# Optimization experiments

Hardware: AMD Instinct MI355X
Metric: run time of the kernel (lower is better)

## Reference

```python
import jax, jax.numpy as jnp
import numpy as np

S, N_SUB, E_SUB = 64, 1024, 16384       # subgraphs, nodes/subgraph, edges/subgraph
N, E = 65536, 1048576                   # global nodes / edges
F_IN, NHID, NCLS, HEADS = 128, 128, 64, 2
RATIO = 0.5
K = int(np.ceil(RATIO * N_SUB))         # SAGPooling keeps K=512 nodes


def setup_inputs() -> dict:
    key = jax.random.key(0)
    ks = jax.random.split(key, 12)
    def lin(k, i, o):
        return jax.random.normal(k, (i, o), jnp.float32) / np.sqrt(i).astype(np.float32)
    return {
        'sub_x': jax.random.normal(ks[0], (S, N_SUB, F_IN), jnp.float32),
        'sub_edge_index': jax.random.randint(ks[1], (S, 2, E_SUB), 0, N_SUB, jnp.int32),
        'sub_orig_idx': jax.random.randint(ks[2], (S, N_SUB), 0, N, jnp.int32),
        'edge_index': jax.random.randint(ks[3], (2, E), 0, N, jnp.int32),
        'W1': lin(ks[4], F_IN, NHID), 'b1': jnp.zeros((NHID,), jnp.float32),
        'W2': lin(ks[5], NHID, NHID), 'b2': jnp.zeros((NHID,), jnp.float32),
        'Wp': lin(ks[6], NHID, 1), 'bp': jnp.zeros((1,), jnp.float32),
        'Wsc': lin(ks[7], NHID, NHID), 'bsc': jnp.zeros((NHID,), jnp.float32),
        'Wqkv': lin(ks[8], 2 * NHID, 6 * NHID), 'bqkv': jnp.zeros((6 * NHID,), jnp.float32),
        'Wo': lin(ks[9], 2 * NHID, 2 * NHID), 'bo': jnp.zeros((2 * NHID,), jnp.float32),
        'Wf': lin(ks[10], 3 * NHID, NCLS), 'bf': jnp.zeros((NCLS,), jnp.float32),
    }


def gcn(x, src, dst, ew, W, b, n):
    """PyG GCNConv: sym-normalized aggregation with self-loops; ew masks invalid edges."""
    h = x @ W
    deg = jax.ops.segment_sum(ew, dst, num_segments=n) + 1.0  # +1 self-loop
    dinv = jax.lax.rsqrt(deg)
    coef = dinv[src] * dinv[dst] * ew
    agg = jax.ops.segment_sum(h[src] * coef[:, None], dst, num_segments=n)
    return agg + h * (dinv * dinv)[:, None] + b


def _forward(sub_x, W1, b1, W2, b2, Wp, bp, Wsc, bsc, Wqkv, bqkv, Wo, bo, Wf, bf,
             sub_edge_index, sub_orig_idx, edge_index):
    dt = sub_x.dtype

    def cacos(x, ei):  # one subgraph: [N_SUB,F], [2,E_SUB]
        src, dst = ei[0], ei[1]
        ew1 = jnp.ones((E_SUB,), dt)
        x1 = jax.nn.relu(gcn(x, src, dst, ew1, W1, b1, N_SUB))
        x2 = jax.nn.relu(gcn(x1, src, dst, ew1, W2, b2, N_SUB))
        # SAGPooling on x1: GCN scorer -> top-k -> tanh gate
        score = gcn(x1, src, dst, ew1, Wp, bp, N_SUB)[:, 0]
        top_s, perm = jax.lax.top_k(score, K)
        x_pool = x1[perm] * jnp.tanh(top_s)[:, None]
        # remap edges to pooled indexing; invalid edges get weight 0
        pos = jnp.full((N_SUB,), -1, jnp.int32).at[perm].set(jnp.arange(K, dtype=jnp.int32))
        valid = (pos[src] >= 0) & (pos[dst] >= 0)
        psrc = jnp.where(valid, pos[src], 0)
        pdst = jnp.where(valid, pos[dst], 0)
        ew2 = valid.astype(dt)
        emb1 = jnp.concatenate([x_pool.max(0), x_pool.mean(0)])  # [2*NHID]
        x_sub = jax.nn.relu(gcn(x_pool, psrc, pdst, ew2, Wsc, bsc, K))
        emb2 = jnp.concatenate([x_sub.max(0), x_sub.mean(0)])
        return x2, emb1 + emb2

    node_embs, sub_embs = jax.vmap(cacos)(sub_x, sub_edge_index)  # [S,N_SUB,NHID], [S,2*NHID]

    # multi-head self-attention over subgraph embeddings (seq_len = 1 per the torch reshape)
    HD = (2 * NHID) // HEADS
    qkv = (sub_embs @ Wqkv + bqkv).reshape(S, 1, 3, HEADS, HD).transpose(2, 0, 3, 1, 4)
    q, k, v = qkv[0], qkv[1], qkv[2]                      # [S,H,1,HD]
    attn = jax.nn.softmax(jnp.einsum('shqd,shkd->shqk', q, k) / np.sqrt(HD).astype(np.float32), axis=-1)
    o = jnp.einsum('shqk,shkd->shqd', attn, v).transpose(0, 2, 1, 3).reshape(S, 1, 2 * NHID)
    att = (o @ Wo + bo)[:, 0]                             # [S, 2*NHID]

    # scatter-add per-node embeddings + broadcast subgraph embedding into global buffer
    combined = jnp.concatenate(
        [node_embs, jnp.broadcast_to(att[:, None, :], (S, N_SUB, 2 * NHID))], axis=-1)
    global_emb = jnp.zeros((N, 3 * NHID), dt).at[sub_orig_idx.reshape(-1)].add(
        combined.reshape(-1, 3 * NHID))

    logits = gcn(global_emb, edge_index[0], edge_index[1], jnp.ones((E,), dt), Wf, bf, N)
    return jax.nn.log_softmax(logits, axis=-1), global_emb


def reference(sub_x, sub_edge_index, sub_orig_idx, edge_index, W1, b1, W2, b2, Wp, bp,
              Wsc, bsc, Wqkv, bqkv, Wo, bo, Wf, bf):
    return _forward(sub_x, W1, b1, W2, b2, Wp, bp, Wsc, bsc, Wqkv, bqkv, Wo, bo, Wf, bf,
                    sub_edge_index, sub_orig_idx, edge_index)
```

## Files before the change

kernel.cpp:

```cpp
#include <hip/hip_runtime.h>
#include <math.h>

#define S     64
#define NSUB  1024
#define ESUB  16384
#define NG    65536
#define EG    1048576
#define NH    128
#define KSEL  512
#define BCAP  20480

__global__ __launch_bounds__(1024) void k_csr_sub(const int* __restrict__ sei,
        const int* __restrict__ sorig, int* __restrict__ rowptr, int* __restrict__ col,
        float* __restrict__ dinv, int* __restrict__ cntR) {
    int b = blockIdx.x, t = threadIdx.x;
    if (b >= 64) {
        int r = (b - 64) * 1024 + t;
        atomicAdd(&cntR[sorig[r]], 1);
        return;
    }
    __shared__ int sh[1024];
    __shared__ int curL[1024];
    int s = b;
    curL[t] = 0;
    __syncthreads();
    const int* dstp = sei + s * 2 * ESUB + ESUB;
    #pragma unroll
    for (int k = 0; k < 16; k++) atomicAdd(&curL[dstp[k * 1024 + t]], 1);
    __syncthreads();
    int v = curL[t];
    sh[t] = v;
    __syncthreads();
    for (int off = 1; off < 1024; off <<= 1) {
        int add = (t >= off) ? sh[t - off] : 0;
        __syncthreads();
        sh[t] += add;
        __syncthreads();
    }
    int incl = sh[t];
    int excl = incl - v;
    rowptr[s * (NSUB + 1) + t] = excl;
    dinv[s * NSUB + t] = rsqrtf((float)(v + 1));
    if (t == 1023) rowptr[s * (NSUB + 1) + NSUB] = incl;
    curL[t] = s * ESUB + excl;
    __syncthreads();
    const int* srcp = sei + s * 2 * ESUB;
    #pragma unroll
    for (int k = 0; k < 16; k++) {
        int e = k * 1024 + t;
        int src = srcp[e];
        int dst = dstp[e];
        int p = atomicAdd(&curL[dst], 1);
        col[p] = src;
    }
}

__global__ __launch_bounds__(1024) void k_scanR(const int* __restrict__ cnt,
        int* __restrict__ rowptr, int* __restrict__ cur) {
    __shared__ int sh[1024];
    __shared__ int wsum[16];
    __shared__ int sboff;
    int b = blockIdx.x, t = threadIdx.x;
    int pre = 0;
    for (int i = t; i < b * 1024; i += 1024) pre += cnt[i];
    #pragma unroll
    for (int o = 32; o > 0; o >>= 1) pre += __shfl_xor(pre, o, 64);
    if ((t & 63) == 0) wsum[t >> 6] = pre;
    __syncthreads();
    if (t == 0) {
        int r = 0;
        #pragma unroll
        for (int i = 0; i < 16; i++) r += wsum[i];
        sboff = r;
    }
    int v = cnt[b * 1024 + t];
    sh[t] = v;
    __syncthreads();
    for (int off = 1; off < 1024; off <<= 1) {
        int add = (t >= off) ? sh[t - off] : 0;
        __syncthreads();
        sh[t] += add;
        __syncthreads();
    }
    int base = sboff;
    int r = base + sh[t] - v;
    int idx = b * 1024 + t;
    rowptr[idx] = r;
    cur[idx] = r;
    if (b == 63 && t == 1023) rowptr[NG] = base + sh[t];
}

__global__ void k_fillR(const int* __restrict__ orig, int* __restrict__ cur,
                        int* __restrict__ rowlist, int* __restrict__ posR) {
    int r = blockIdx.x * 256 + threadIdx.x;
    int p = atomicAdd(&cur[orig[r]], 1);
    rowlist[p] = r;
    posR[r] = p;
}

template<int KDIM, int NCOL>
__global__ __launch_bounds__(256) void k_matmul(const float* __restrict__ X,
        const float* __restrict__ W, float* __restrict__ Y) {
    __shared__ float As[16][72];
    __shared__ float Bs[16][72];
    int t = threadIdx.x;
    int row0 = blockIdx.x * 64;
    int col0 = blockIdx.y * 64;
    int tr = t >> 4, tc = t & 15;
    float acc[4][4] = {};
    for (int k0 = 0; k0 < KDIM; k0 += 16) {
        {   int r = t >> 2, kq = t & 3;
            float4 v = *(const float4*)&X[(size_t)(row0 + r) * KDIM + k0 + kq * 4];
            As[kq * 4 + 0][r] = v.x; As[kq * 4 + 1][r] = v.y;
            As[kq * 4 + 2][r] = v.z; As[kq * 4 + 3][r] = v.w;
        }
        {   int k = t >> 4, cq = t & 15;
            float4 v = *(const float4*)&W[(size_t)(k0 + k) * NCOL + col0 + cq * 4];
            *(float4*)&Bs[k][cq * 4] = v;
        }
        __syncthreads();
        #pragma unroll
        for (int k = 0; k < 16; k++) {
            float a0 = As[k][tr * 4 + 0], a1 = As[k][tr * 4 + 1];
            float a2 = As[k][tr * 4 + 2], a3 = As[k][tr * 4 + 3];
            float b0 = Bs[k][tc * 4 + 0], b1 = Bs[k][tc * 4 + 1];
            float b2 = Bs[k][tc * 4 + 2], b3 = Bs[k][tc * 4 + 3];
            acc[0][0] += a0 * b0; acc[0][1] += a0 * b1; acc[0][2] += a0 * b2; acc[0][3] += a0 * b3;
            acc[1][0] += a1 * b0; acc[1][1] += a1 * b1; acc[1][2] += a1 * b2; acc[1][3] += a1 * b3;
            acc[2][0] += a2 * b0; acc[2][1] += a2 * b1; acc[2][2] += a2 * b2; acc[2][3] += a2 * b3;
            acc[3][0] += a3 * b0; acc[3][1] += a3 * b1; acc[3][2] += a3 * b2; acc[3][3] += a3 * b3;
        }
        __syncthreads();
    }
    #pragma unroll
    for (int i = 0; i < 4; i++) {
        float4 v = { acc[i][0], acc[i][1], acc[i][2], acc[i][3] };
        *(float4*)&Y[(size_t)(row0 + tr * 4 + i) * NCOL + col0 + tc * 4] = v;
    }
}

__global__ __launch_bounds__(256) void k_mm2s(const float* __restrict__ X,
        const float* __restrict__ W, float* __restrict__ Y,
        const float* __restrict__ sh, const float* __restrict__ dinv,
        const int* __restrict__ rowptr, const int* __restrict__ col,
        const float* __restrict__ bp, float* __restrict__ score) {
    int t = threadIdx.x;
    if (blockIdx.x >= 2048) {
        int n = (blockIdx.x - 2048) * 256 + t;
        int s = n >> 10, nl = n & (NSUB - 1);
        const int* rp = rowptr + s * (NSUB + 1);
        const int* cl = col + s * ESUB;
        const float* dv = dinv + s * NSUB;
        int st = rp[nl], en = rp[nl + 1];
        float acc = 0.f;
        for (int p = st; p < en; p++) {
            int src = cl[p];
            acc += sh[s * NSUB + src] * dv[src];
        }
        float dn = dv[nl];
        score[n] = acc * dn + sh[n] * dn * dn + bp[0];
        return;
    }
    __shared__ float As[16][72];
    __shared__ float Bs[16][72];
    int row0 = (blockIdx.x & 1023) * 64;
    int col0 = (blockIdx.x >> 10) * 64;
    int tr = t >> 4, tc = t & 15;
    float acc[4][4] = {};
    for (int k0 = 0; k0 < 128; k0 += 16) {
        {   int r = t >> 2, kq = t & 3;
            float4 v = *(const float4*)&X[(size_t)(row0 + r) * 128 + k0 + kq * 4];
            As[kq * 4 + 0][r] = v.x; As[kq * 4 + 1][r] = v.y;
            As[kq * 4 + 2][r] = v.z; As[kq * 4 + 3][r] = v.w;
        }
        {   int k = t >> 4, cq = t & 15;
            float4 v = *(const float4*)&W[(size_t)(k0 + k) * 128 + col0 + cq * 4];
            *(float4*)&Bs[k][cq * 4] = v;
        }
        __syncthreads();
        #pragma unroll
        for (int k = 0; k < 16; k++) {
            float a0 = As[k][tr * 4 + 0], a1 = As[k][tr * 4 + 1];
            float a2 = As[k][tr * 4 + 2], a3 = As[k][tr * 4 + 3];
            float b0 = Bs[k][tc * 4 + 0], b1 = Bs[k][tc * 4 + 1];
            float b2 = Bs[k][tc * 4 + 2], b3 = Bs[k][tc * 4 + 3];
            acc[0][0] += a0 * b0; acc[0][1] += a0 * b1; acc[0][2] += a0 * b2; acc[0][3] += a0 * b3;
            acc[1][0] += a1 * b0; acc[1][1] += a1 * b1; acc[1][2] += a1 * b2; acc[1][3] += a1 * b3;
            acc[2][0] += a2 * b0; acc[2][1] += a2 * b1; acc[2][2] += a2 * b2; acc[2][3] += a2 * b3;
            acc[3][0] += a3 * b0; acc[3][1] += a3 * b1; acc[3][2] += a3 * b2; acc[3][3] += a3 * b3;
        }
        __syncthreads();
    }
    #pragma unroll
    for (int i = 0; i < 4; i++) {
        float4 v = { acc[i][0], acc[i][1], acc[i][2], acc[i][3] };
        *(float4*)&Y[(size_t)(row0 + tr * 4 + i) * 128 + col0 + tc * 4] = v;
    }
}

template<bool SCORE, bool SCATTER>
__global__ __launch_bounds__(256) void k_agg128(const float4* __restrict__ h,
        const float* __restrict__ dinv, const int* __restrict__ rowptr,
        const int* __restrict__ col, const float* __restrict__ bias,
        const float* __restrict__ Wp, const int* __restrict__ posR,
        float4* __restrict__ out, float* __restrict__ scoreh) {
    int b = blockIdx.x;
    int s = b & 63;
    int chunk = b >> 6;
    int t = threadIdx.x;
    int nl = chunk * 8 + (t >> 5);
    int f4 = t & 31;
    const int* rp = rowptr + s * (NSUB + 1);
    int st = rp[nl], en = rp[nl + 1];
    const int* cl = col + s * ESUB;
    const float* dv = dinv + s * NSUB;
    float4 acc = {0.f, 0.f, 0.f, 0.f};
    for (int p = st; p < en; p++) {
        int src = cl[p];
        float d = dv[src];
        float4 hv = h[((size_t)(s * NSUB + src)) * 32 + f4];
        acc.x += hv.x * d; acc.y += hv.y * d; acc.z += hv.z * d; acc.w += hv.w * d;
    }
    size_t node = (size_t)s * NSUB + nl;
    float dn = dv[nl];
    float dn2 = dn * dn;
    float4 hs = h[node * 32 + f4];
    float4 bb = ((const float4*)bias)[f4];
    float4 r;
    r.x = fmaxf(acc.x * dn + hs.x * dn2 + bb.x, 0.f);
    r.y = fmaxf(acc.y * dn + hs.y * dn2 + bb.y, 0.f);
    r.z = fmaxf(acc.z * dn + hs.z * dn2 + bb.z, 0.f);
    r.w = fmaxf(acc.w * dn + hs.w * dn2 + bb.w, 0.f);
    size_t orow = SCATTER ? (size_t)posR[node] : node;
    out[orow * 32 + f4] = r;
    if (SCORE) {
        float4 wp = ((const float4*)Wp)[f4];
        float p = r.x * wp.x + r.y * wp.y + r.z * wp.z + r.w * wp.w;
        #pragma unroll
        for (int o = 16; o > 0; o >>= 1) p += __shfl_xor(p, o, 32);
        if (f4 == 0) scoreh[node] = p;
    }
}

__global__ __launch_bounds__(512) void k_topk(const float* __restrict__ score,
        int* __restrict__ perm, float* __restrict__ gate, int* __restrict__ posmap) {
    __shared__ float sv[1024];
    __shared__ int   si[1024];
    int s = blockIdx.x, t = threadIdx.x;
    for (int i = t; i < 1024; i += 512) {
        sv[i] = score[s * NSUB + i];
        si[i] = i;
        posmap[s * NSUB + i] = -1;
    }
    __syncthreads();
    for (int k = 2; k <= 1024; k <<= 1) {
        for (int j = k >> 1; j > 0; j >>= 1) {
            for (int b = t; b < 1024; b += 512) {
                int ixj = b ^ j;
                if (ixj > b) {
                    bool desc = ((b & k) == 0);
                    bool sw = desc ? (sv[b] < sv[ixj]) : (sv[b] > sv[ixj]);
                    if (sw) {
                        float tv = sv[b]; sv[b] = sv[ixj]; sv[ixj] = tv;
                        int ti = si[b]; si[b] = si[ixj]; si[ixj] = ti;
                    }
                }
            }
            __syncthreads();
        }
    }
    if (t < KSEL) {
        perm[s * KSEL + t] = si[t];
        gate[s * KSEL + t] = tanhf(sv[t]);
        posmap[s * NSUB + si[t]] = t;
    }
}

__global__ __launch_bounds__(256) void k_pool(const float4* __restrict__ x1,
        const int* __restrict__ perm, const float* __restrict__ gate,
        const int* __restrict__ posmap, const int* __restrict__ rowptr,
        const int* __restrict__ col, float* __restrict__ dinv2,
        float4* __restrict__ xpool) {
    int t = threadIdx.x;
    int i = blockIdx.x * 8 + (t >> 5);
    int lane = t & 31;
    int s = i >> 9;
    int n = perm[i];
    const int* rp = rowptr + s * (NSUB + 1);
    const int* cl = col + s * ESUB;
    int st = rp[n], en = rp[n + 1];
    int c = 0;
    for (int p = st + lane; p < en; p += 32) c += (posmap[s * NSUB + cl[p]] >= 0) ? 1 : 0;
    #pragma unroll
    for (int o = 16; o > 0; o >>= 1) c += __shfl_xor(c, o, 32);
    if (lane == 0) dinv2[i] = rsqrtf((float)(c + 1));
    float g = gate[i];
    float4 v = x1[((size_t)(s * NSUB + n)) * 32 + lane];
    v.x *= g; v.y *= g; v.z *= g; v.w *= g;
    xpool[(size_t)i * 32 + lane] = v;
}

__global__ __launch_bounds__(1024) void k_emb(const float* __restrict__ X,
        float* __restrict__ out) {
    __shared__ float red[4][256];
    int s = blockIdx.x, t = threadIdx.x;
    int sl = t >> 8, f = t & 255;
    const float* base = X + (size_t)s * KSEL * NH;
    float r;
    if (f < NH) {
        r = -INFINITY;
        for (int i = sl * 128; i < sl * 128 + 128; i++) r = fmaxf(r, base[i * NH + f]);
    } else {
        r = 0.f;
        for (int i = sl * 128; i < sl * 128 + 128; i++) r += base[i * NH + (f - NH)];
    }
    red[sl][f] = r;
    __syncthreads();
    if (sl == 0) {
        float a = red[0][f], b = red[1][f], c = red[2][f], d = red[3][f];
        float v = (f < NH) ? fmaxf(fmaxf(a, b), fmaxf(c, d)) : (a + b + c + d) * (1.f / KSEL);
        out[s * 256 + f] = v;
    }
}

__global__ __launch_bounds__(256) void k_aggp_bin(const float4* __restrict__ hp,
        const float* __restrict__ dinv2, const int* __restrict__ perm,
        const int* __restrict__ posmap, const int* __restrict__ rowptr,
        const int* __restrict__ col, const float* __restrict__ bsc,
        float4* __restrict__ xsub,
        const int* __restrict__ gei, int* __restrict__ bcur, int* __restrict__ ebin) {
    int t = threadIdx.x;
    if (blockIdx.x >= 4096) {
        __shared__ int lh[64];
        __shared__ int lbase[64];
        if (t < 64) lh[t] = 0;
        __syncthreads();
        int e0 = (blockIdx.x - 4096) * 8192;
        #pragma unroll 8
        for (int k = 0; k < 32; k++) {
            int d = gei[EG + e0 + k * 256 + t];
            atomicAdd(&lh[d >> 10], 1);
        }
        __syncthreads();
        if (t < 64) {
            lbase[t] = t * BCAP + atomicAdd(&bcur[t], lh[t]);
            lh[t] = 0;
        }
        __syncthreads();
        #pragma unroll 4
        for (int k = 0; k < 32; k++) {
            int idx = e0 + k * 256 + t;
            int d = gei[EG + idx];
            int src = gei[idx];
            int bb = d >> 10;
            int pos = lbase[bb] + atomicAdd(&lh[bb], 1);
            ebin[pos] = src | ((d & 1023) << 16);
        }
        return;
    }
    int b = blockIdx.x;
    int s = b & 63;
    int chunk = b >> 6;
    int il = chunk * 8 + (t >> 5);
    int f4 = t & 31;
    int i = s * KSEL + il;
    int n = perm[i];
    const int* rp = rowptr + s * (NSUB + 1);
    const int* cl = col + s * ESUB;
    int st = rp[n], en = rp[n + 1];
    float4 acc = {0.f, 0.f, 0.f, 0.f};
    for (int p = st; p < en; p++) {
        int j = posmap[s * NSUB + cl[p]];
        if (j >= 0) {
            float d = dinv2[s * KSEL + j];
            float4 hv = hp[((size_t)(s * KSEL + j)) * 32 + f4];
            acc.x += hv.x * d; acc.y += hv.y * d; acc.z += hv.z * d; acc.w += hv.w * d;
        }
    }
    float dn = dinv2[i];
    float dn2 = dn * dn;
    float4 hs = hp[(size_t)i * 32 + f4];
    float4 bb = ((const float4*)bsc)[f4];
    float4 r;
    r.x = fmaxf(acc.x * dn + hs.x * dn2 + bb.x, 0.f);
    r.y = fmaxf(acc.y * dn + hs.y * dn2 + bb.y, 0.f);
    r.z = fmaxf(acc.z * dn + hs.z * dn2 + bb.z, 0.f);
    r.w = fmaxf(acc.w * dn + hs.w * dn2 + bb.w, 0.f);
    xsub[(size_t)i * 32 + f4] = r;
}

__global__ __launch_bounds__(1024) void k_ea_fb(const float* __restrict__ X,
        const float* __restrict__ subemb, const float* __restrict__ Wqkv,
        const float* __restrict__ bqkv, const float* __restrict__ Wo,
        const float* __restrict__ bo, const float* __restrict__ Wf,
        float* __restrict__ att, float* __restrict__ AW,
        const int* __restrict__ ebin, const int* __restrict__ bcur,
        int* __restrict__ rowptrN, float* __restrict__ dinvN, int* __restrict__ colN) {
    int t = threadIdx.x;
    if (blockIdx.x >= 64) {
        __shared__ int sh2[1024];
        __shared__ int curL[1024];
        __shared__ int sbase;
        int b = blockIdx.x - 64;
        if (t == 0) {
            int run = 0;
            for (int i = 0; i < b; i++) run += bcur[i];
            sbase = run;
        }
        curL[t] = 0;
        __syncthreads();
        int st = b * BCAP, en = st + bcur[b];
        for (int i = st + t; i < en; i += 1024) atomicAdd(&curL[ebin[i] >> 16], 1);
        __syncthreads();
        int v = curL[t];
        sh2[t] = v;
        __syncthreads();
        for (int off = 1; off < 1024; off <<= 1) {
            int add = (t >= off) ? sh2[t - off] : 0;
            __syncthreads();
            sh2[t] += add;
            __syncthreads();
        }
        int incl = sh2[t];
        int excl = incl - v;
        int base = sbase;
        rowptrN[(b << 10) + t] = base + excl;
        dinvN[(b << 10) + t] = rsqrtf((float)(v + 1));
        if (b == 63 && t == 1023) rowptrN[NG] = base + incl;
        curL[t] = base + excl;
        __syncthreads();
        for (int i = st + t; i < en; i += 1024) {
            int packed = ebin[i];
            int p = atomicAdd(&curL[packed >> 16], 1);
            colN[p] = packed & 0xFFFF;
        }
        return;
    }
    __shared__ float red[4][256];
    __shared__ float se[256], t1[256], av[256];
    int s = blockIdx.x;
    int sl = t >> 8, f = t & 255;
    const float* base = X + (size_t)s * KSEL * NH;
    float r;
    if (f < NH) {
        r = -INFINITY;
        for (int i = sl * 128; i < sl * 128 + 128; i++) r = fmaxf(r, base[i * NH + f]);
    } else {
        r = 0.f;
        for (int i = sl * 128; i < sl * 128 + 128; i++) r += base[i * NH + (f - NH)];
    }
    red[sl][f] = r;
    __syncthreads();
    if (sl == 0) {
        float a = red[0][f], b = red[1][f], c = red[2][f], d = red[3][f];
        float v = (f < NH) ? fmaxf(fmaxf(a, b), fmaxf(c, d)) : (a + b + c + d) * (1.f / KSEL);
        se[f] = subemb[s * 256 + f] + v;
    }
    __syncthreads();
    if (sl == 0) {
        float acc = bqkv[512 + f];
        for (int k = 0; k < 256; k++) acc += se[k] * Wqkv[(size_t)k * 768 + 512 + f];
        t1[f] = acc;
    }
    __syncthreads();
    if (sl == 0) {
        float a2 = bo[f];
        for (int k = 0; k < 256; k++) a2 += t1[k] * Wo[(size_t)k * 256 + f];
        att[s * 256 + f] = a2;
        av[f] = a2;
    }
    __syncthreads();
    if (sl == 0 && f < 64) {
        float acc = 0.f;
        for (int k = 0; k < 256; k++) acc += av[k] * Wf[(size_t)(NH + k) * 64 + f];
        AW[s * 64 + f] = acc;
    }
}

__global__ __launch_bounds__(256) void k_gx(const float4* __restrict__ x2s,
        const float4* __restrict__ att, const int* __restrict__ rowptrR,
        const int* __restrict__ rowlist, float4* __restrict__ gemb,
        const float* __restrict__ X, const float* __restrict__ W,
        const float* __restrict__ AW, float* __restrict__ Y) {
    int t = threadIdx.x;
    if (blockIdx.x < NG / 8) {
        int g = blockIdx.x * 8 + (t >> 5);
        int lane = t & 31;
        int st = rowptrR[g], en = rowptrR[g + 1];
        float4 a0 = {0.f,0.f,0.f,0.f}, a1 = {0.f,0.f,0.f,0.f}, a2 = {0.f,0.f,0.f,0.f};
        for (int p = st; p < en; p++) {
            float4 v = x2s[(size_t)p * 32 + lane];
            a0.x += v.x; a0.y += v.y; a0.z += v.z; a0.w += v.w;
            int sub = rowlist[p] >> 10;
            float4 w1 = att[(size_t)sub * 64 + lane];
            float4 w2 = att[(size_t)sub * 64 + 32 + lane];
            a1.x += w1.x; a1.y += w1.y; a1.z += w1.z; a1.w += w1.w;
            a2.x += w2.x; a2.y += w2.y; a2.z += w2.z; a2.w += w2.w;
        }
        gemb[(size_t)g * 96 + lane]      = a0;
        gemb[(size_t)g * 96 + 32 + lane] = a1;
        gemb[(size_t)g * 96 + 64 + lane] = a2;
        return;
    }
    __shared__ float As[16][72];
    __shared__ float Bs[16][72];
    int row0 = (blockIdx.x - NG / 8) * 64;
    int tr = t >> 4, tc = t & 15;
    float acc[4][4] = {};
    for (int k0 = 0; k0 < 128; k0 += 16) {
        {   int r = t >> 2, kq = t & 3;
            float4 v = *(const float4*)&X[(size_t)(row0 + r) * 128 + k0 + kq * 4];
            As[kq * 4 + 0][r] = v.x; As[kq * 4 + 1][r] = v.y;
            As[kq * 4 + 2][r] = v.z; As[kq * 4 + 3][r] = v.w;
        }
        {   int k = t >> 4, cq = t & 15;
            float4 v = *(const float4*)&W[(size_t)(k0 + k) * 64 + cq * 4];
            *(float4*)&Bs[k][cq * 4] = v;
        }
        __syncthreads();
        #pragma unroll
        for (int k = 0; k < 16; k++) {
            float a0 = As[k][tr * 4 + 0], a1 = As[k][tr * 4 + 1];
            float a2 = As[k][tr * 4 + 2], a3 = As[k][tr * 4 + 3];
            float b0 = Bs[k][tc * 4 + 0], b1 = Bs[k][tc * 4 + 1];
            float b2 = Bs[k][tc * 4 + 2], b3 = Bs[k][tc * 4 + 3];
            acc[0][0] += a0 * b0; acc[0][1] += a0 * b1; acc[0][2] += a0 * b2; acc[0][3] += a0 * b3;
            acc[1][0] += a1 * b0; acc[1][1] += a1 * b1; acc[1][2] += a1 * b2; acc[1][3] += a1 * b3;
            acc[2][0] += a2 * b0; acc[2][1] += a2 * b1; acc[2][2] += a2 * b2; acc[2][3] += a2 * b3;
            acc[3][0] += a3 * b0; acc[3][1] += a3 * b1; acc[3][2] += a3 * b2; acc[3][3] += a3 * b3;
        }
        __syncthreads();
    }
    #pragma unroll
    for (int i = 0; i < 4; i++) {
        int rr = row0 + tr * 4 + i;
        int sub = rowlist[rr] >> 10;
        const float4 aw = *(const float4*)&AW[(size_t)sub * 64 + tc * 4];
        float4 v = { acc[i][0] + aw.x, acc[i][1] + aw.y, acc[i][2] + aw.z, acc[i][3] + aw.w };
        *(float4*)&Y[(size_t)rr * 64 + tc * 4] = v;
    }
}

__global__ __launch_bounds__(256) void k_gatherH(const float4* __restrict__ X2Ws,
        const int* __restrict__ rowptrR, float4* __restrict__ hf) {
    int t = threadIdx.x;
    int g = blockIdx.x * 16 + (t >> 4);
    int f4 = t & 15;
    int st = rowptrR[g], en = rowptrR[g + 1];
    float4 acc = {0.f, 0.f, 0.f, 0.f};
    for (int p = st; p < en; p++) {
        float4 a = X2Ws[(size_t)p * 16 + f4];
        acc.x += a.x; acc.y += a.y; acc.z += a.z; acc.w += a.w;
    }
    hf[(size_t)g * 16 + f4] = acc;
}

__global__ __launch_bounds__(256) void k_final(const float4* __restrict__ hf,
        const float* __restrict__ dinvN, const int* __restrict__ rowptr,
        const int* __restrict__ col, const float* __restrict__ bfb,
        float4* __restrict__ out) {
    int t = threadIdx.x;
    int n = blockIdx.x * 16 + (t >> 4);
    int f4 = t & 15;
    int st = rowptr[n], en = rowptr[n + 1];
    float4 acc = {0.f, 0.f, 0.f, 0.f};
    for (int p = st; p < en; p++) {
        int src = col[p];
        float d = dinvN[src];
        float4 hv = hf[(size_t)src * 16 + f4];
        acc.x += hv.x * d; acc.y += hv.y * d; acc.z += hv.z * d; acc.w += hv.w * d;
    }
    float dn = dinvN[n];
    float dn2 = dn * dn;
    float4 hs = hf[(size_t)n * 16 + f4];
    float4 bb = ((const float4*)bfb)[f4];
    float4 x;
    x.x = acc.x * dn + hs.x * dn2 + bb.x;
    x.y = acc.y * dn + hs.y * dn2 + bb.y;
    x.z = acc.z * dn + hs.z * dn2 + bb.z;
    x.w = acc.w * dn + hs.w * dn2 + bb.w;
    float m = fmaxf(fmaxf(x.x, x.y), fmaxf(x.z, x.w));
    for (int o = 1; o < 16; o <<= 1) m = fmaxf(m, __shfl_xor(m, o, 64));
    float ssum = expf(x.x - m) + expf(x.y - m) + expf(x.z - m) + expf(x.w - m);
    for (int o = 1; o < 16; o <<= 1) ssum += __shfl_xor(ssum, o, 64);
    float lz = m + logf(ssum);
    float4 r = { x.x - lz, x.y - lz, x.z - lz, x.w - lz };
    out[(size_t)n * 16 + f4] = r;
}

extern "C" void kernel_launch(void* const* d_in, const int* in_sizes, int n_in,
                              void* d_out, int out_size, void* d_ws, size_t ws_size,
                              hipStream_t stream) {
    const float* sub_x = (const float*)d_in[0];
    const int*   sei   = (const int*)d_in[1];
    const int*   sorig = (const int*)d_in[2];
    const int*   gei   = (const int*)d_in[3];
    const float *W1 = (const float*)d_in[4],  *b1  = (const float*)d_in[5];
    const float *W2 = (const float*)d_in[6],  *b2  = (const float*)d_in[7];
    const float *Wp = (const float*)d_in[8],  *bp  = (const float*)d_in[9];
    const float *Wsc = (const float*)d_in[10], *bsc = (const float*)d_in[11];
    const float *Wqkv = (const float*)d_in[12], *bqkv = (const float*)d_in[13];
    const float *Wo = (const float*)d_in[14], *bo  = (const float*)d_in[15];
    const float *Wf = (const float*)d_in[16], *bfb = (const float*)d_in[17];

    float* out0 = (float*)d_out;
    float* gemb = (float*)d_out + (size_t)NG * 64;

    char* w = (char*)d_ws;
    size_t off = 0;
    auto alloc = [&](size_t nbytes) -> void* {
        off = (off + 255) & ~(size_t)255;
        void* p = w + off;
        off += nbytes;
        return p;
    };
    int*   bcur    = (int*)alloc(64 * 4);
    int*   cntR    = (int*)alloc((size_t)NG * 4);
    float* AW      = (float*)alloc((size_t)S * 64 * 4);
    float* dinv    = (float*)alloc((size_t)NG * 4);
    float* scoreh  = (float*)alloc((size_t)NG * 4);
    float* score   = (float*)alloc((size_t)NG * 4);
    float* gate    = (float*)alloc((size_t)S * KSEL * 4);
    float* dinv2   = (float*)alloc((size_t)S * KSEL * 4);
    float* subemb  = (float*)alloc((size_t)S * 256 * 4);
    float* att     = (float*)alloc((size_t)S * 256 * 4);
    int*   perm    = (int*)alloc((size_t)S * KSEL * 4);
    int*   posmap  = (int*)alloc((size_t)NG * 4);
    int*   cur_sub = (int*)alloc((size_t)NG * 4);
    int*   rowptr_s= (int*)alloc((size_t)(NG + 64) * 4);
    int*   col_sub = (int*)alloc((size_t)EG * 4);
    int*   rowptrR = (int*)alloc((size_t)(NG + 64) * 4);
    int*   rowlist = (int*)alloc((size_t)NG * 4);
    int*   posR    = (int*)alloc((size_t)NG * 4);
    float* x1      = (float*)alloc((size_t)NG * NH * 4);
    float* x2s     = (float*)alloc((size_t)NG * NH * 4);
    float* hbuf    = (float*)alloc((size_t)NG * NH * 4);
    float* xpool   = (float*)alloc((size_t)S * KSEL * NH * 4);
    float* xsub    = x1;
    float* hf      = hbuf;
    float* dinvN   = dinv;
    float* X2Ws    = x1;
    int*   curR    = cur_sub;
    int*   rowptrN = rowptr_s;
    int*   colN    = col_sub;
    int*   ebin    = (int*)xpool;

    hipMemsetAsync(bcur, 0, 256 + (size_t)NG * 4, stream);

    k_csr_sub<<<128, 1024, 0, stream>>>(sei, sorig, rowptr_s, col_sub, dinv, cntR);
    k_scanR<<<64, 1024, 0, stream>>>(cntR, rowptrR, curR);
    k_fillR<<<NG / 256, 256, 0, stream>>>(sorig, curR, rowlist, posR);

    k_matmul<128, 128><<<dim3(NG / 64, 2), 256, 0, stream>>>(sub_x, W1, hbuf);
    k_agg128<true, false><<<8192, 256, 0, stream>>>((const float4*)hbuf, dinv, rowptr_s,
                                                    col_sub, b1, Wp, nullptr, (float4*)x1, scoreh);
    k_mm2s<<<2048 + NG / 256, 256, 0, stream>>>(x1, W2, hbuf,
                                                scoreh, dinv, rowptr_s, col_sub, bp, score);
    k_agg128<false, true><<<8192, 256, 0, stream>>>((const float4*)hbuf, dinv, rowptr_s,
                                                    col_sub, b2, nullptr, posR, (float4*)x2s, nullptr);
    k_topk<<<S, 512, 0, stream>>>(score, perm, gate, posmap);
    k_pool<<<(S * KSEL) / 8, 256, 0, stream>>>((const float4*)x1, perm, gate, posmap,
                                               rowptr_s, col_sub, dinv2, (float4*)xpool);
    k_emb<<<S, 1024, 0, stream>>>(xpool, subemb);
    k_matmul<128, 128><<<dim3((S * KSEL) / 64, 2), 256, 0, stream>>>(xpool, Wsc, hbuf);
    k_aggp_bin<<<4096 + EG / 8192, 256, 0, stream>>>((const float4*)hbuf, dinv2, perm, posmap,
                                                     rowptr_s, col_sub, bsc, (float4*)xsub,
                                                     gei, bcur, ebin);
    k_ea_fb<<<128, 1024, 0, stream>>>(xsub, subemb, Wqkv, bqkv, Wo, bo, Wf, att, AW,
                                      ebin, bcur, rowptrN, dinvN, colN);
    k_gx<<<NG / 8 + NG / 64, 256, 0, stream>>>((const float4*)x2s, (const float4*)att,
                                               rowptrR, rowlist, (float4*)gemb,
                                               x2s, Wf, AW, X2Ws);
    k_gatherH<<<NG / 16, 256, 0, stream>>>((const float4*)X2Ws, rowptrR, (float4*)hf);

    k_final<<<NG / 16, 256, 0, stream>>>((const float4*)hf, dinvN, rowptrN, colN, bfb, (float4*)out0);

    (void)in_sizes; (void)n_in; (void)out_size; (void)ws_size;
}
```

Before: 682.1 us.

## Fold independent stages into shared launches to cut kernel count

The first matmul (sub_x·W1) is split across the CSR-build and scan launches as extra 1024-thread blocks computing 128x128 tiles, so independent work shares those launches. The top-k sort is merged into the second aggregation launch as extra blocks, and the pooled-feature matmul is merged with the embedding reduction. This removes several launches and lets independent stages overlap, at the cost of larger, heterogeneous blocks whose shared memory use and 1024-thread size may reduce occupancy for the matmul and aggregation parts.

```diff
diff --git a/kernel.cpp b/kernel.cpp
--- a/kernel.cpp
+++ b/kernel.cpp
@@ -10,113 +10,21 @@
 #define KSEL  512
 #define BCAP  20480
 
-__global__ __launch_bounds__(1024) void k_csr_sub(const int* __restrict__ sei,
-        const int* __restrict__ sorig, int* __restrict__ rowptr, int* __restrict__ col,
-        float* __restrict__ dinv, int* __restrict__ cntR) {
-    int b = blockIdx.x, t = threadIdx.x;
-    if (b >= 64) {
-        int r = (b - 64) * 1024 + t;
-        atomicAdd(&cntR[sorig[r]], 1);
-        return;
-    }
-    __shared__ int sh[1024];
-    __shared__ int curL[1024];
-    int s = b;
-    curL[t] = 0;
-    __syncthreads();
-    const int* dstp = sei + s * 2 * ESUB + ESUB;
-    #pragma unroll
-    for (int k = 0; k < 16; k++) atomicAdd(&curL[dstp[k * 1024 + t]], 1);
-    __syncthreads();
-    int v = curL[t];
-    sh[t] = v;
-    __syncthreads();
-    for (int off = 1; off < 1024; off <<= 1) {
-        int add = (t >= off) ? sh[t - off] : 0;
-        __syncthreads();
-        sh[t] += add;
-        __syncthreads();
-    }
-    int incl = sh[t];
-    int excl = incl - v;
-    rowptr[s * (NSUB + 1) + t] = excl;
-    dinv[s * NSUB + t] = rsqrtf((float)(v + 1));
-    if (t == 1023) rowptr[s * (NSUB + 1) + NSUB] = incl;
-    curL[t] = s * ESUB + excl;
-    __syncthreads();
-    const int* srcp = sei + s * 2 * ESUB;
-    #pragma unroll
-    for (int k = 0; k < 16; k++) {
-        int e = k * 1024 + t;
-        int src = srcp[e];
-        int dst = dstp[e];
-        int p = atomicAdd(&curL[dst], 1);
-        col[p] = src;
-    }
-}
-
-__global__ __launch_bounds__(1024) void k_scanR(const int* __restrict__ cnt,
-        int* __restrict__ rowptr, int* __restrict__ cur) {
-    __shared__ int sh[1024];
-    __shared__ int wsum[16];
-    __shared__ int sboff;
-    int b = blockIdx.x, t = threadIdx.x;
-    int pre = 0;
-    for (int i = t; i < b * 1024; i += 1024) pre += cnt[i];
-    #pragma unroll
-    for (int o = 32; o > 0; o >>= 1) pre += __shfl_xor(pre, o, 64);
-    if ((t & 63) == 0) wsum[t >> 6] = pre;
-    __syncthreads();
-    if (t == 0) {
-        int r = 0;
-        #pragma unroll
-        for (int i = 0; i < 16; i++) r += wsum[i];
-        sboff = r;
-    }
-    int v = cnt[b * 1024 + t];
-    sh[t] = v;
-    __syncthreads();
-    for (int off = 1; off < 1024; off <<= 1) {
-        int add = (t >= off) ? sh[t - off] : 0;
-        __syncthreads();
-        sh[t] += add;
-        __syncthreads();
-    }
-    int base = sboff;
-    int r = base + sh[t] - v;
-    int idx = b * 1024 + t;
-    rowptr[idx] = r;
-    cur[idx] = r;
-    if (b == 63 && t == 1023) rowptr[NG] = base + sh[t];
-}
-
-__global__ void k_fillR(const int* __restrict__ orig, int* __restrict__ cur,
-                        int* __restrict__ rowlist, int* __restrict__ posR) {
-    int r = blockIdx.x * 256 + threadIdx.x;
-    int p = atomicAdd(&cur[orig[r]], 1);
-    rowlist[p] = r;
-    posR[r] = p;
-}
-
-template<int KDIM, int NCOL>
-__global__ __launch_bounds__(256) void k_matmul(const float* __restrict__ X,
-        const float* __restrict__ W, float* __restrict__ Y) {
-    __shared__ float As[16][72];
-    __shared__ float Bs[16][72];
-    int t = threadIdx.x;
-    int row0 = blockIdx.x * 64;
-    int col0 = blockIdx.y * 64;
-    int tr = t >> 4, tc = t & 15;
+__device__ __forceinline__ void mm1024_tile(const float* __restrict__ X,
+        const float* __restrict__ W, float* __restrict__ Y, int row0, int t,
+        float (*As)[136], float (*Bs)[136]) {
+    int tr = t >> 5, tc = t & 31;
     float acc[4][4] = {};
-    for (int k0 = 0; k0 < KDIM; k0 += 16) {
-        {   int r = t >> 2, kq = t & 3;
-            float4 v = *(const float4*)&X[(size_t)(row0 + r) * KDIM + k0 + kq * 4];
+    for (int k0 = 0; k0 < 128; k0 += 16) {
+        if (t < 512) {
+            int r = t >> 2, kq = t & 3;
+            float4 v = *(const float4*)&X[(size_t)(row0 + r) * 128 + k0 + kq * 4];
             As[kq * 4 + 0][r] = v.x; As[kq * 4 + 1][r] = v.y;
             As[kq * 4 + 2][r] = v.z; As[kq * 4 + 3][r] = v.w;
-        }
-        {   int k = t >> 4, cq = t & 15;
-            float4 v = *(const float4*)&W[(size_t)(k0 + k) * NCOL + col0 + cq * 4];
-            *(float4*)&Bs[k][cq * 4] = v;
+        } else {
+            int u = t - 512;
+            int k = u >> 5, c = (u & 31) * 4;
+            *(float4*)&Bs[k][c] = *(const float4*)&W[(size_t)(k0 + k) * 128 + c];
         }
         __syncthreads();
         #pragma unroll
@@ -135,8 +43,110 @@
     #pragma unroll
     for (int i = 0; i < 4; i++) {
         float4 v = { acc[i][0], acc[i][1], acc[i][2], acc[i][3] };
-        *(float4*)&Y[(size_t)(row0 + tr * 4 + i) * NCOL + col0 + tc * 4] = v;
-    }
+        *(float4*)&Y[(size_t)(row0 + tr * 4 + i) * 128 + tc * 4] = v;
+    }
+}
+
+__global__ __launch_bounds__(1024) void k_csr_mm1(const int* __restrict__ sei,
+        const int* __restrict__ sorig, int* __restrict__ rowptr, int* __restrict__ col,
+        float* __restrict__ dinv, int* __restrict__ cntR,
+        const float* __restrict__ X, const float* __restrict__ W, float* __restrict__ Y) {
+    __shared__ float As[16][136];
+    __shared__ float Bs[16][136];
+    __shared__ int sh[1024];
+    __shared__ int curL[1024];
+    int b = blockIdx.x, t = threadIdx.x;
+    if (b >= 128) {
+        mm1024_tile(X, W, Y, (b - 128) * 128, t, As, Bs);
+        return;
+    }
+    if (b >= 64) {
+        int r = (b - 64) * 1024 + t;
+        atomicAdd(&cntR[sorig[r]], 1);
+        return;
+    }
+    int s = b;
+    curL[t] = 0;
+    __syncthreads();
+    const int* dstp = sei + s * 2 * ESUB + ESUB;
+    #pragma unroll
+    for (int k = 0; k < 16; k++) atomicAdd(&curL[dstp[k * 1024 + t]], 1);
+    __syncthreads();
+    int v = curL[t];
+    sh[t] = v;
+    __syncthreads();
+    for (int off = 1; off < 1024; off <<= 1) {
+        int add = (t >= off) ? sh[t - off] : 0;
+        __syncthreads();
+        sh[t] += add;
+        __syncthreads();
+    }
+    int incl = sh[t];
+    int excl = incl - v;
+    rowptr[s * (NSUB + 1) + t] = excl;
+    dinv[s * NSUB + t] = rsqrtf((float)(v + 1));
+    if (t == 1023) rowptr[s * (NSUB + 1) + NSUB] = incl;
+    curL[t] = s * ESUB + excl;
+    __syncthreads();
+    const int* srcp = sei + s * 2 * ESUB;
+    #pragma unroll
+    for (int k = 0; k < 16; k++) {
+        int e = k * 1024 + t;
+        int src = srcp[e];
+        int dst = dstp[e];
+        int p = atomicAdd(&curL[dst], 1);
+        col[p] = src;
+    }
+}
+
+__global__ __launch_bounds__(1024) void k_scan_mm1(const int* __restrict__ cnt,
+        int* __restrict__ rowptr, int* __restrict__ cur,
+        const float* __restrict__ X, const float* __restrict__ W, float* __restrict__ Y) {
+    __shared__ float As[16][136];
+    __shared__ float Bs[16][136];
+    __shared__ int sh[1024];
+    __shared__ int wsum[16];
+    __shared__ int sboff;
+    int b = blockIdx.x, t = threadIdx.x;
+    if (b >= 64) {
+        mm1024_tile(X, W, Y, (b - 64 + 256) * 128, t, As, Bs);
+        return;
+    }
+    int pre = 0;
+    for (int i = t; i < b * 1024; i += 1024) pre += cnt[i];
+    #pragma unroll
+    for (int o = 32; o > 0; o >>= 1) pre += __shfl_xor(pre, o, 64);
+    if ((t & 63) == 0) wsum[t >> 6] = pre;
+    __syncthreads();
+    if (t == 0) {
+        int r = 0;
+        #pragma unroll
+        for (int i = 0; i < 16; i++) r += wsum[i];
+        sboff = r;
+    }
+    int v = cnt[b * 1024 + t];
+    sh[t] = v;
+    __syncthreads();
+    for (int off = 1; off < 1024; off <<= 1) {
+        int add = (t >= off) ? sh[t - off] : 0;
+        __syncthreads();
+        sh[t] += add;
+        __syncthreads();
+    }
+    int base = sboff;
+    int r = base + sh[t] - v;
+    int idx = b * 1024 + t;
+    rowptr[idx] = r;
+    cur[idx] = r;
+    if (b == 63 && t == 1023) rowptr[NG] = base + sh[t];
+}
+
+__global__ void k_fillR(const int* __restrict__ orig, int* __restrict__ cur,
+                        int* __restrict__ rowlist, int* __restrict__ posR) {
+    int r = blockIdx.x * 256 + threadIdx.x;
+    int p = atomicAdd(&cur[orig[r]], 1);
+    rowlist[p] = r;
+    posR[r] = p;
 }
 
 __global__ __launch_bounds__(256) void k_mm2s(const float* __restrict__ X,
@@ -198,12 +208,11 @@
     }
 }
 
-template<bool SCORE, bool SCATTER>
-__global__ __launch_bounds__(256) void k_agg128(const float4* __restrict__ h,
+__global__ __launch_bounds__(256) void k_agg1(const float4* __restrict__ h,
         const float* __restrict__ dinv, const int* __restrict__ rowptr,
         const int* __restrict__ col, const float* __restrict__ bias,
-        const float* __restrict__ Wp, const int* __restrict__ posR,
-        float4* __restrict__ out, float* __restrict__ scoreh) {
+        const float* __restrict__ Wp, float4* __restrict__ out,
+        float* __restrict__ scoreh) {
     int b = blockIdx.x;
     int s = b & 63;
     int chunk = b >> 6;
@@ -231,49 +240,81 @@
     r.y = fmaxf(acc.y * dn + hs.y * dn2 + bb.y, 0.f);
     r.z = fmaxf(acc.z * dn + hs.z * dn2 + bb.z, 0.f);
     r.w = fmaxf(acc.w * dn + hs.w * dn2 + bb.w, 0.f);
-    size_t orow = SCATTER ? (size_t)posR[node] : node;
-    out[orow * 32 + f4] = r;
-    if (SCORE) {
-        float4 wp = ((const float4*)Wp)[f4];
-        float p = r.x * wp.x + r.y * wp.y + r.z * wp.z + r.w * wp.w;
-        #pragma unroll
-        for (int o = 16; o > 0; o >>= 1) p += __shfl_xor(p, o, 32);
-        if (f4 == 0) scoreh[node] = p;
-    }
-}
-
-__global__ __launch_bounds__(512) void k_topk(const float* __restrict__ score,
-        int* __restrict__ perm, float* __restrict__ gate, int* __restrict__ posmap) {
-    __shared__ float sv[1024];
-    __shared__ int   si[1024];
-    int s = blockIdx.x, t = threadIdx.x;
-    for (int i = t; i < 1024; i += 512) {
-        sv[i] = score[s * NSUB + i];
-        si[i] = i;
-        posmap[s * NSUB + i] = -1;
-    }
-    __syncthreads();
-    for (int k = 2; k <= 1024; k <<= 1) {
-        for (int j = k >> 1; j > 0; j >>= 1) {
-            for (int b = t; b < 1024; b += 512) {
-                int ixj = b ^ j;
-                if (ixj > b) {
-                    bool desc = ((b & k) == 0);
-                    bool sw = desc ? (sv[b] < sv[ixj]) : (sv[b] > sv[ixj]);
-                    if (sw) {
-                        float tv = sv[b]; sv[b] = sv[ixj]; sv[ixj] = tv;
-                        int ti = si[b]; si[b] = si[ixj]; si[ixj] = ti;
+    out[node * 32 + f4] = r;
+    float4 wp = ((const float4*)Wp)[f4];
+    float p = r.x * wp.x + r.y * wp.y + r.z * wp.z + r.w * wp.w;
+    #pragma unroll
+    for (int o = 16; o > 0; o >>= 1) p += __shfl_xor(p, o, 32);
+    if (f4 == 0) scoreh[node] = p;
+}
+
+__global__ __launch_bounds__(512) void k_agg2_topk(const float4* __restrict__ h,
+        const float* __restrict__ dinv, const int* __restrict__ rowptr,
+        const int* __restrict__ col, const float* __restrict__ bias,
+        const int* __restrict__ posR, float4* __restrict__ out,
+        const float* __restrict__ score, int* __restrict__ perm,
+        float* __restrict__ gate, int* __restrict__ posmap) {
+    int t = threadIdx.x;
+    if (blockIdx.x >= 4096) {
+        __shared__ float sv[1024];
+        __shared__ int   si[1024];
+        int s = blockIdx.x - 4096;
+        for (int i = t; i < 1024; i += 512) {
+            sv[i] = score[s * NSUB + i];
+            si[i] = i;
+            posmap[s * NSUB + i] = -1;
+        }
+        __syncthreads();
+        for (int k = 2; k <= 1024; k <<= 1) {
+            for (int j = k >> 1; j > 0; j >>= 1) {
+                for (int b = t; b < 1024; b += 512) {
+                    int ixj = b ^ j;
+                    if (ixj > b) {
+                        bool desc = ((b & k) == 0);
+                        bool sw = desc ? (sv[b] < sv[ixj]) : (sv[b] > sv[ixj]);
+                        if (sw) {
+                            float tv = sv[b]; sv[b] = sv[ixj]; sv[ixj] = tv;
+                            int ti = si[b]; si[b] = si[ixj]; si[ixj] = ti;
+                        }
                     }
                 }
+                __syncthreads();
             }
-            __syncthreads();
-        }
-    }
-    if (t < KSEL) {
-        perm[s * KSEL + t] = si[t];
-        gate[s * KSEL + t] = tanhf(sv[t]);
-        posmap[s * NSUB + si[t]] = t;
-    }
+        }
+        if (t < KSEL) {
+            perm[s * KSEL + t] = si[t];
+            gate[s * KSEL + t] = tanhf(sv[t]);
+            posmap[s * NSUB + si[t]] = t;
+        }
+        return;
+    }
+    int b = blockIdx.x;
+    int s = b & 63;
+    int chunk = b >> 6;
+    int nl = chunk * 16 + (t >> 5);
+    int f4 = t & 31;
+    const int* rp = rowptr + s * (NSUB + 1);
+    int st = rp[nl], en = rp[nl + 1];
+    const int* cl = col + s * ESUB;
+    const float* dv = dinv + s * NSUB;
+    float4 acc = {0.f, 0.f, 0.f, 0.f};
+    for (int p = st; p < en; p++) {
+        int src = cl[p];
+        float d = dv[src];
+        float4 hv = h[((size_t)(s * NSUB + src)) * 32 + f4];
+        acc.x += hv.x * d; acc.y += hv.y * d; acc.z += hv.z * d; acc.w += hv.w * d;
+    }
+    size_t node = (size_t)s * NSUB + nl;
+    float dn = dv[nl];
+    float dn2 = dn * dn;
+    float4 hs = h[node * 32 + f4];
+    float4 bb = ((const float4*)bias)[f4];
+    float4 r;
+    r.x = fmaxf(acc.x * dn + hs.x * dn2 + bb.x, 0.f);
+    r.y = fmaxf(acc.y * dn + hs.y * dn2 + bb.y, 0.f);
+    r.z = fmaxf(acc.z * dn + hs.z * dn2 + bb.z, 0.f);
+    r.w = fmaxf(acc.w * dn + hs.w * dn2 + bb.w, 0.f);
+    out[(size_t)posR[node] * 32 + f4] = r;
 }
 
 __global__ __launch_bounds__(256) void k_pool(const float4* __restrict__ x1,
@@ -300,10 +341,17 @@
     xpool[(size_t)i * 32 + lane] = v;
 }
 
-__global__ __launch_bounds__(1024) void k_emb(const float* __restrict__ X,
-        float* __restrict__ out) {
+__global__ __launch_bounds__(1024) void k_emb_mmP(const float* __restrict__ X,
+        float* __restrict__ out, const float* __restrict__ W, float* __restrict__ Y) {
+    __shared__ float As[16][136];
+    __shared__ float Bs[16][136];
     __shared__ float red[4][256];
-    int s = blockIdx.x, t = threadIdx.x;
+    int b = blockIdx.x, t = threadIdx.x;
+    if (b >= 64) {
+        mm1024_tile(X, W, Y, (b - 64) * 128, t, As, Bs);
+        return;
+    }
+    int s = b;
     int sl = t >> 8, f = t & 255;
     const float* base = X + (size_t)s * KSEL * NH;
     float r;
@@ -317,8 +365,8 @@
     red[sl][f] = r;
     __syncthreads();
     if (sl == 0) {
-        float a = red[0][f], b = red[1][f], c = red[2][f], d = red[3][f];
-        float v = (f < NH) ? fmaxf(fmaxf(a, b), fmaxf(c, d)) : (a + b + c + d) * (1.f / KSEL);
+        float a = red[0][f], bb = red[1][f], c = red[2][f], d = red[3][f];
+        float v = (f < NH) ? fmaxf(fmaxf(a, bb), fmaxf(c, d)) : (a + bb + c + d) * (1.f / KSEL);
         out[s * 256 + f] = v;
     }
 }
@@ -647,22 +695,21 @@
 
     hipMemsetAsync(bcur, 0, 256 + (size_t)NG * 4, stream);
 
-    k_csr_sub<<<128, 1024, 0, stream>>>(sei, sorig, rowptr_s, col_sub, dinv, cntR);
-    k_scanR<<<64, 1024, 0, stream>>>(cntR, rowptrR, curR);
+    k_csr_mm1<<<384, 1024, 0, stream>>>(sei, sorig, rowptr_s, col_sub, dinv, cntR,
+                                        sub_x, W1, hbuf);
+    k_scan_mm1<<<320, 1024, 0, stream>>>(cntR, rowptrR, curR, sub_x, W1, hbuf);
     k_fillR<<<NG / 256, 256, 0, stream>>>(sorig, curR, rowlist, posR);
 
-    k_matmul<128, 128><<<dim3(NG / 64, 2), 256, 0, stream>>>(sub_x, W1, hbuf);
-    k_agg128<true, false><<<8192, 256, 0, stream>>>((const float4*)hbuf, dinv, rowptr_s,
-                                                    col_sub, b1, Wp, nullptr, (float4*)x1, scoreh);
+    k_agg1<<<8192, 256, 0, stream>>>((const float4*)hbuf, dinv, rowptr_s, col_sub,
+                                     b1, Wp, (float4*)x1, scoreh);
     k_mm2s<<<2048 + NG / 256, 256, 0, stream>>>(x1, W2, hbuf,
                                                 scoreh, dinv, rowptr_s, col_sub, bp, score);
-    k_agg128<false, true><<<8192, 256, 0, stream>>>((const float4*)hbuf, dinv, rowptr_s,
-                                                    col_sub, b2, nullptr, posR, (float4*)x2s, nullptr);
-    k_topk<<<S, 512, 0, stream>>>(score, perm, gate, posmap);
+    k_agg2_topk<<<4096 + S, 512, 0, stream>>>((const float4*)hbuf, dinv, rowptr_s, col_sub,
+                                              b2, posR, (float4*)x2s,
+                                              score, perm, gate, posmap);
     k_pool<<<(S * KSEL) / 8, 256, 0, stream>>>((const float4*)x1, perm, gate, posmap,
                                                rowptr_s, col_sub, dinv2, (float4*)xpool);
-    k_emb<<<S, 1024, 0, stream>>>(xpool, subemb);
-    k_matmul<128, 128><<<dim3((S * KSEL) / 64, 2), 256, 0, stream>>>(xpool, Wsc, hbuf);
+    k_emb_mmP<<<64 + (S * KSEL) / 128, 1024, 0, stream>>>(xpool, subemb, Wsc, hbuf);
     k_aggp_bin<<<4096 + EG / 8192, 256, 0, stream>>>((const float4*)hbuf, dinv2, perm, posmap,
                                                      rowptr_s, col_sub, bsc, (float4*)xsub,
                                                      gei, bcur, ebin);
```

Result: faster. 663.6 us (-2.7%).
